# Optimization experiments

Measured on AMD Instinct MI355X. Metric: run time of the kernel, lower is better.

## Reference

```python
import jax, jax.numpy as jnp
import numpy as np

D_MODEL = 1024

def setup_inputs() -> dict:
    key = jax.random.key(0)
    ks = jax.random.split(key, 7)
    B, S, D = 4, 2048, D_MODEL
    scale = 1.0 / np.sqrt(D)
    x = jax.random.normal(ks[0], (B, S, D), dtype=jnp.float32)
    Wq = jax.random.normal(ks[1], (D, D), dtype=jnp.float32) * scale
    bq = jnp.zeros((D,), dtype=jnp.float32)
    Wk = jax.random.normal(ks[2], (D, D), dtype=jnp.float32) * scale
    bk = jnp.zeros((D,), dtype=jnp.float32)
    Wv = jax.random.normal(ks[3], (D, D), dtype=jnp.float32) * scale
    bv = jnp.zeros((D,), dtype=jnp.float32)
    return {"x": x, "Wq": Wq, "bq": bq, "Wk": Wk, "bk": bk, "Wv": Wv, "bv": bv}

def reference(x, Wq, bq, Wk, bk, Wv, bv):
    # Single-head attention; scale = 1/sqrt(d_model) as in the torch module (self.d_k = d_model).
    d_k = x.shape[-1]
    q = jnp.einsum('bsd,de->bse', x, Wq) + bq
    k = jnp.einsum('bsd,de->bse', x, Wk) + bk
    v = jnp.einsum('bsd,de->bse', x, Wv) + bv
    scores = jnp.einsum('bqd,bkd->bqk', q, k) / jnp.sqrt(jnp.asarray(d_k, x.dtype))
    attn = jax.nn.softmax(scores, axis=-1)
    return jnp.einsum('bqk,bkd->bqd', attn, v)
```

## Files before the change

### kernel.cpp

```cpp
#include <hip/hip_runtime.h>
#include <hip/hip_bf16.h>

#define DM 1024
#define SEQ 2048
#define NBATCH 4

using f32x4 = __attribute__((ext_vector_type(4))) float;
using s16x8 = __attribute__((ext_vector_type(8))) short;
using u16x4 = __attribute__((ext_vector_type(4))) unsigned short;
using u16x8 = __attribute__((ext_vector_type(8))) unsigned short;

__device__ __forceinline__ unsigned short f2bf(float f) {
  union { float f; unsigned u; } v; v.f = f;
  return (unsigned short)((v.u + 0x7fffu + ((v.u >> 16) & 1u)) >> 16);
}

__device__ __forceinline__ void g2lds16(const void* g, void* l) {
  __builtin_amdgcn_global_load_lds(
      (const __attribute__((address_space(1))) void*)g,
      (__attribute__((address_space(3))) void*)l, 16, 0, 0);
}


__global__ void cvt_x(const float* __restrict__ X, unsigned short* __restrict__ XB) {
  const int i = blockIdx.x * 256 + threadIdx.x;
  const f32x4* p = (const f32x4*)X;
  f32x4 a = p[2 * i], b = p[2 * i + 1];
  u16x8 o;
#pragma unroll
  for (int q = 0; q < 4; q++) { o[q] = f2bf(a[q]); o[4 + q] = f2bf(b[q]); }
  *(u16x8*)(XB + (size_t)i * 8) = o;
}

__global__ void transpose_w(const float* __restrict__ Wq, const float* __restrict__ Wk,
                            const float* __restrict__ Wv, unsigned short* __restrict__ WT) {
  const int seg = blockIdx.z;
  const float* W = (seg == 0) ? Wq : (seg == 1) ? Wk : Wv;
  unsigned short* out = WT + (size_t)seg * DM * DM;
  __shared__ float t[32][33];
  const int k0 = blockIdx.y * 32, n0 = blockIdx.x * 32;
  const int tr = threadIdx.x >> 5, tc = threadIdx.x & 31;
#pragma unroll
  for (int p = 0; p < 4; p++) {
    int r = tr + p * 8;
    t[r][tc] = W[(size_t)(k0 + r) * DM + n0 + tc];
  }
  __syncthreads();
#pragma unroll
  for (int p = 0; p < 4; p++) {
    int r = tr + p * 8;
    out[(size_t)(n0 + r) * DM + k0 + tc] = f2bf(t[tc][r]);
  }
}

template <int MODE, int LDA, int LDB, int KDIM>
__global__ void gemm_nt(const unsigned short* __restrict__ A,
                        const unsigned short* __restrict__ B,
                        void* __restrict__ C0,
                        unsigned short* __restrict__ C1,
                        unsigned short* __restrict__ C2,
                        const float* __restrict__ bq,
                        const float* __restrict__ bk,
                        const float* __restrict__ bv) {
  __shared__ unsigned short lA[128 * 64];
  __shared__ unsigned short lB[128 * 64];

  const int tid = threadIdx.x;
  const int w = tid >> 6;
  const int L = tid & 63;
  const int wm = w & 1, wn = w >> 1;
  const int bz = blockIdx.z;
  const int tileM = blockIdx.y * 128, tileN = blockIdx.x * 128;

  const unsigned short* Ab = A;
  const unsigned short* Bb = B;
  if (MODE == 1) { Ab += (size_t)bz * SEQ * DM; Bb += (size_t)bz * SEQ * DM; }
  if (MODE == 2) { Ab += (size_t)bz * SEQ * SEQ; Bb += (size_t)bz * DM * SEQ; }

  const int srow = tid >> 3;
  const int gchunk = (tid & 7) ^ (srow & 7);
  const char* gA0 = (const char*)(Ab + (size_t)(tileM + srow) * LDA) + gchunk * 16;
  const char* gB0 = (const char*)(Bb + (size_t)(tileN + srow) * LDB) + gchunk * 16;
  const size_t strA32 = (size_t)32 * LDA * 2;
  const size_t strB32 = (size_t)32 * LDB * 2;
  char* lAw = (char*)lA + w * 1024;
  char* lBw = (char*)lB + w * 1024;

  f32x4 acc[4][4];
#pragma unroll
  for (int i = 0; i < 4; i++)
#pragma unroll
    for (int j = 0; j < 4; j++) acc[i][j] = (f32x4){0.f, 0.f, 0.f, 0.f};

  const int rl = L & 15;
  const int qh = L >> 4;
  const int sw = L & 7;

  for (int k = 0; k < KDIM; k += 64) {
    const size_t kb = (size_t)k * 2;
#pragma unroll
    for (int c = 0; c < 4; c++) {
      g2lds16(gA0 + c * strA32 + kb, lAw + c * 4096);
      g2lds16(gB0 + c * strB32 + kb, lBw + c * 4096);
    }
    __syncthreads();

#pragma unroll
    for (int s = 0; s < 2; s++) {
      const int pc = ((s * 4 + qh) ^ sw) * 8;
      s16x8 av[4], bv4[4];
#pragma unroll
      for (int i = 0; i < 4; i++)
        av[i] = *(const s16x8*)&lA[(wm * 64 + i * 16 + rl) * 64 + pc];
#pragma unroll
      for (int j = 0; j < 4; j++)
        bv4[j] = *(const s16x8*)&lB[(wn * 64 + j * 16 + rl) * 64 + pc];
#pragma unroll
      for (int i = 0; i < 4; i++)
#pragma unroll
        for (int j = 0; j < 4; j++)
          acc[i][j] = __builtin_amdgcn_mfma_f32_16x16x32_bf16(av[i], bv4[j], acc[i][j], 0, 0, 0);
    }
    __syncthreads();
  }

#pragma unroll
  for (int i = 0; i < 4; i++) {
    const int gm0 = tileM + wm * 64 + i * 16 + (L >> 4) * 4;
#pragma unroll
    for (int j = 0; j < 4; j++) {
      const int gn = tileN + wn * 64 + j * 16 + (L & 15);
      if (MODE == 0) {
        const int seg = gn >> 10;
        const int colin = gn & 1023;
        if (seg == 0) {
          const float bias = bq[colin];
          unsigned short* Q = (unsigned short*)C0;
#pragma unroll
          for (int r = 0; r < 4; r++) Q[(size_t)(gm0 + r) * DM + colin] = f2bf(acc[i][j][r] + bias);
        } else if (seg == 1) {
          const float bias = bk[colin];
#pragma unroll
          for (int r = 0; r < 4; r++) C1[(size_t)(gm0 + r) * DM + colin] = f2bf(acc[i][j][r] + bias);
        } else {
          const float bias = bv[colin];
          u16x4 pk;
#pragma unroll
          for (int r = 0; r < 4; r++) pk[r] = f2bf(acc[i][j][r] + bias);
          const int b = gm0 >> 11, s0 = gm0 & 2047;
          *(u16x4*)(C2 + ((size_t)((b << 10) + colin)) * SEQ + s0) = pk;
        }
      } else if (MODE == 1) {
        float* S = (float*)C0 + (size_t)bz * SEQ * SEQ;
#pragma unroll
        for (int r = 0; r < 4; r++) S[(size_t)(gm0 + r) * SEQ + gn] = acc[i][j][r] * 0.03125f;
      } else {
        float* O = (float*)C0 + (size_t)bz * SEQ * DM;
#pragma unroll
        for (int r = 0; r < 4; r++) O[(size_t)(gm0 + r) * DM + gn] = acc[i][j][r];
      }
    }
  }
}

__global__ void softmax_k(const float* __restrict__ S, unsigned short* __restrict__ P) {
  const int row = blockIdx.x;
  const float* src = S + (size_t)row * SEQ;
  const int t = threadIdx.x;
  f32x4 a = *(const f32x4*)(src + t * 8);
  f32x4 b = *(const f32x4*)(src + t * 8 + 4);
  float m = fmaxf(fmaxf(fmaxf(a[0], a[1]), fmaxf(a[2], a[3])),
                  fmaxf(fmaxf(b[0], b[1]), fmaxf(b[2], b[3])));
#pragma unroll
  for (int o = 32; o > 0; o >>= 1) m = fmaxf(m, __shfl_down(m, o, 64));
  __shared__ float redm[4], reds[4];
  if ((t & 63) == 0) redm[t >> 6] = m;
  __syncthreads();
  m = fmaxf(fmaxf(redm[0], redm[1]), fmaxf(redm[2], redm[3]));
  float e[8]; float s = 0.f;
#pragma unroll
  for (int q = 0; q < 4; q++) { e[q] = __expf(a[q] - m); s += e[q]; }
#pragma unroll
  for (int q = 0; q < 4; q++) { e[4 + q] = __expf(b[q] - m); s += e[4 + q]; }
#pragma unroll
  for (int o = 32; o > 0; o >>= 1) s += __shfl_down(s, o, 64);
  if ((t & 63) == 0) reds[t >> 6] = s;
  __syncthreads();
  s = reds[0] + reds[1] + reds[2] + reds[3];
  const float inv = 1.0f / s;
  u16x8 o8;
#pragma unroll
  for (int q = 0; q < 8; q++) o8[q] = f2bf(e[q] * inv);
  *(u16x8*)(P + (size_t)row * SEQ + t * 8) = o8;
}

extern "C" void kernel_launch(void* const* d_in, const int* in_sizes, int n_in,
                              void* d_out, int out_size, void* d_ws, size_t ws_size,
                              hipStream_t stream) {
  (void)in_sizes; (void)n_in; (void)out_size; (void)ws_size;
  const float* x  = (const float*)d_in[0];
  const float* Wq = (const float*)d_in[1];
  const float* bq = (const float*)d_in[2];
  const float* Wk = (const float*)d_in[3];
  const float* bk = (const float*)d_in[4];
  const float* Wv = (const float*)d_in[5];
  const float* bv = (const float*)d_in[6];
  float* out = (float*)d_out;
  char* ws = (char*)d_ws;
  unsigned short* xb = (unsigned short*)(ws + 0);
  unsigned short* wt = (unsigned short*)(ws + 16777216);
  unsigned short* qb = (unsigned short*)(ws + 23068672);
  unsigned short* kb = (unsigned short*)(ws + 39845888);
  unsigned short* vt = (unsigned short*)(ws + 56623104);
  float*          S  = (float*)         (ws + 73400320);
  unsigned short* P  = (unsigned short*)(ws + 140509184);

  cvt_x<<<4096, 256, 0, stream>>>(x, xb);
  transpose_w<<<dim3(32, 32, 3), 256, 0, stream>>>(Wq, Wk, Wv, wt);
  gemm_nt<0, 1024, 1024, 1024><<<dim3(24, 64, 1), 256, 0, stream>>>(
      xb, wt, (void*)qb, kb, vt, bq, bk, bv);
  gemm_nt<1, 1024, 1024, 1024><<<dim3(16, 16, 4), 256, 0, stream>>>(
      qb, kb, (void*)S, nullptr, nullptr, nullptr, nullptr, nullptr);
  softmax_k<<<8192, 256, 0, stream>>>(S, P);
  gemm_nt<2, 2048, 2048, 2048><<<dim3(8, 16, 4), 256, 0, stream>>>(
      P, vt, (void*)out, nullptr, nullptr, nullptr, nullptr, nullptr);
}
```

Baseline: 269.7 us.

## Prefetch next K tile into registers while computing current tile in GEMM

Replaces direct global-to-LDS loads with a register-staged software pipeline. The next K tile is loaded into registers before the MFMA work on the current tile, then written to LDS after a barrier. This is meant to hide global memory latency behind compute without adding LDS. The cost is more VGPR pressure, an extra barrier per iteration, and explicit LDS stores in place of the async global_load_lds path.

```diff
diff --git a/kernel.cpp b/kernel.cpp
--- a/kernel.cpp
+++ b/kernel.cpp
@@ -13,12 +13,6 @@
 __device__ __forceinline__ unsigned short f2bf(float f) {
   union { float f; unsigned u; } v; v.f = f;
   return (unsigned short)((v.u + 0x7fffu + ((v.u >> 16) & 1u)) >> 16);
-}
-
-__device__ __forceinline__ void g2lds16(const void* g, void* l) {
-  __builtin_amdgcn_global_load_lds(
-      (const __attribute__((address_space(1))) void*)g,
-      (__attribute__((address_space(3))) void*)l, 16, 0, 0);
 }
 
 
@@ -78,13 +72,29 @@
   if (MODE == 2) { Ab += (size_t)bz * SEQ * SEQ; Bb += (size_t)bz * DM * SEQ; }
 
   const int srow = tid >> 3;
-  const int gchunk = (tid & 7) ^ (srow & 7);
-  const char* gA0 = (const char*)(Ab + (size_t)(tileM + srow) * LDA) + gchunk * 16;
-  const char* gB0 = (const char*)(Bb + (size_t)(tileN + srow) * LDB) + gchunk * 16;
-  const size_t strA32 = (size_t)32 * LDA * 2;
-  const size_t strB32 = (size_t)32 * LDB * 2;
-  char* lAw = (char*)lA + w * 1024;
-  char* lBw = (char*)lB + w * 1024;
+  const int pch = tid & 7;
+  const int gch = pch ^ (srow & 7);
+  const unsigned short* gA = Ab + (size_t)(tileM + srow) * LDA + gch * 8;
+  const unsigned short* gB = Bb + (size_t)(tileN + srow) * LDB + gch * 8;
+  unsigned short* wA = &lA[srow * 64 + pch * 8];
+  unsigned short* wB = &lB[srow * 64 + pch * 8];
+
+  u16x8 rA[4], rB[4];
+#define LOADT(kt) do {                                                         \
+    const size_t kk_ = (size_t)(kt) * 64;                                      \
+    _Pragma("unroll")                                                          \
+    for (int i_ = 0; i_ < 4; i_++) {                                           \
+      rA[i_] = *(const u16x8*)(gA + (size_t)i_ * 32 * LDA + kk_);              \
+      rB[i_] = *(const u16x8*)(gB + (size_t)i_ * 32 * LDB + kk_);              \
+    }                                                                          \
+  } while (0)
+#define WRITET() do {                                                          \
+    _Pragma("unroll")                                                          \
+    for (int i_ = 0; i_ < 4; i_++) {                                           \
+      *(u16x8*)(wA + i_ * 32 * 64) = rA[i_];                                   \
+      *(u16x8*)(wB + i_ * 32 * 64) = rB[i_];                                   \
+    }                                                                          \
+  } while (0)
 
   f32x4 acc[4][4];
 #pragma unroll
@@ -96,14 +106,13 @@
   const int qh = L >> 4;
   const int sw = L & 7;
 
-  for (int k = 0; k < KDIM; k += 64) {
-    const size_t kb = (size_t)k * 2;
-#pragma unroll
-    for (int c = 0; c < 4; c++) {
-      g2lds16(gA0 + c * strA32 + kb, lAw + c * 4096);
-      g2lds16(gB0 + c * strB32 + kb, lBw + c * 4096);
-    }
-    __syncthreads();
+  constexpr int NK = KDIM / 64;
+  LOADT(0);
+  WRITET();
+  __syncthreads();
+
+  for (int k = 0; k < NK; ++k) {
+    if (k + 1 < NK) LOADT(k + 1);
 
 #pragma unroll
     for (int s = 0; s < 2; s++) {
@@ -121,8 +130,18 @@
         for (int j = 0; j < 4; j++)
           acc[i][j] = __builtin_amdgcn_mfma_f32_16x16x32_bf16(av[i], bv4[j], acc[i][j], 0, 0, 0);
     }
-    __syncthreads();
-  }
+
+    if (k + 1 < NK) {
+      __builtin_amdgcn_s_waitcnt(0xC07F);
+      __builtin_amdgcn_sched_barrier(0);
+      __builtin_amdgcn_s_barrier();
+      __builtin_amdgcn_sched_barrier(0);
+      WRITET();
+      __syncthreads();
+    }
+  }
+#undef LOADT
+#undef WRITET
 
 #pragma unroll
   for (int i = 0; i < 4; i++) {
```

After: 267.8 us. Within noise of the previous version (-0.7%).
